# Kernel optimization log

Hardware: AMD Instinct MI355X
Metric: run time of the kernel (lower is better)

Reference implementation:

```python
import jax, jax.numpy as jnp
import numpy as np

N = 100000   # nodes
E = 1600000  # edges (avg degree 16)
F_IN = 128
H = 128
C = 16


def setup_inputs() -> dict:
    key = jax.random.key(0)
    ks = jax.random.split(key, 13)
    s = 1.0 / np.sqrt(H)
    return {
        "x": jax.random.normal(ks[0], (N, F_IN), jnp.float32),
        "edge_index": jax.random.randint(ks[1], (2, E), 0, N, jnp.int32),
        "edge_weight": jax.random.uniform(ks[2], (E,), jnp.float32),
        "W1": jax.random.normal(ks[3], (F_IN, H), jnp.float32) * s,
        "b1": jnp.zeros((H,), jnp.float32),
        "W2": jax.random.normal(ks[4], (H, H), jnp.float32) * s,
        "b2": jnp.zeros((H,), jnp.float32),
        "Wg": jax.random.normal(ks[5], (H, H), jnp.float32) * s,
        "att_src": jax.random.normal(ks[6], (H,), jnp.float32) * s,
        "att_dst": jax.random.normal(ks[7], (H,), jnp.float32) * s,
        "bg": jnp.zeros((H,), jnp.float32),
        "Wc": jax.random.normal(ks[8], (H, C), jnp.float32) * s,
        "bc": jnp.zeros((C,), jnp.float32),
    }


def reference(x, edge_index, edge_weight, W1, b1, W2, b2, Wg, att_src, att_dst, bg, Wc, bc):
    n = x.shape[0]
    loop = jnp.arange(n, dtype=edge_index.dtype)
    src = jnp.concatenate([edge_index[0], loop])   # self loops (PyG default)
    dst = jnp.concatenate([edge_index[1], loop])
    ew = jnp.concatenate([edge_weight, jnp.ones((n,), x.dtype)])  # loop weight 1

    # GCN normalization: D^{-1/2} A D^{-1/2}, degree on dst with edge weights
    deg = jax.ops.segment_sum(ew, dst, num_segments=n)
    dinv = jnp.where(deg > 0, jax.lax.rsqrt(deg), 0.0)
    norm = dinv[src] * ew * dinv[dst]              # [E+N]

    def gcn(h, W, b):
        h = h @ W                                   # [N,H]
        agg = jax.ops.segment_sum(h[src] * norm[:, None], dst, num_segments=n)
        return agg + b

    h = jax.nn.relu(gcn(x, W1, b1))
    h = jax.nn.relu(gcn(h, W2, b2))                 # dropout inert in eval

    # GATConv, heads=1
    g = h @ Wg                                      # [N,H]
    a = jax.nn.leaky_relu((g @ att_src)[src] + (g @ att_dst)[dst], 0.2)
    amax = jax.ops.segment_max(a, dst, num_segments=n)
    ex = jnp.exp(a - amax[dst])
    denom = jax.ops.segment_sum(ex, dst, num_segments=n)
    alpha = ex / denom[dst]                         # edge softmax per dst
    out = jax.ops.segment_sum(g[src] * alpha[:, None], dst, num_segments=n) + bg
    out = jax.nn.relu(out)
    return out @ Wc + bc
```

## Files before the change

### kernel.cpp

```cpp
#include <hip/hip_runtime.h>
#include <hip/hip_fp16.h>

#define FIN 128
#define HD 128
#define COUT 16

#define SLOT_CAP 48
#define CS_BLOCKS 512
#define CB_SHIFT 9
#define CB_SIZE 512
#define CAP_B 10240
#define GMK_CELLS 64
#define NBINS 49

typedef _Float16 half8 __attribute__((ext_vector_type(8)));
typedef float floatx4 __attribute__((ext_vector_type(4)));

__device__ __forceinline__ float lrelu02(float x) { return x > 0.f ? x : 0.2f * x; }

union U4H8 { uint4 q; __half2 h2[4]; };
union UQH8 { uint4 q; half8 h; _Float16 e[8]; };

__device__ __forceinline__ void h8f(const uint4 q, float* f) {
    U4H8 u; u.q = q;
    float2 a0 = __half22float2(u.h2[0]);
    float2 a1 = __half22float2(u.h2[1]);
    float2 a2 = __half22float2(u.h2[2]);
    float2 a3 = __half22float2(u.h2[3]);
    f[0] = a0.x; f[1] = a0.y; f[2] = a1.x; f[3] = a1.y;
    f[4] = a2.x; f[5] = a2.y; f[6] = a3.x; f[7] = a3.y;
}

__device__ __forceinline__ unsigned fkey(float f) {
    unsigned u = __float_as_uint(f);
    return (u & 0x80000000u) ? ~u : (u | 0x80000000u);
}
__device__ __forceinline__ float funkey(unsigned k) {
    return (k & 0x80000000u) ? __uint_as_float(k ^ 0x80000000u)
                             : __uint_as_float(~k);
}

__global__ void k_setup(const float* __restrict__ W1, const float* __restrict__ W2,
                        const float* __restrict__ Wg, __half* __restrict__ w1z,
                        __half* __restrict__ w2z, __half* __restrict__ wgz,
                        int* __restrict__ cur, unsigned* __restrict__ gmk,
                        int* __restrict__ hist) {
    int b = blockIdx.x;
    if (b < 24) {
        const float* W = (b < 8) ? W1 : (b < 16) ? W2 : Wg;
        __half* outp   = (b < 8) ? w1z : (b < 16) ? w2z : wgz;
        int t = (b & 7) * 256 + threadIdx.x;
        int lane = t & 63;
        int kc = (t >> 6) & 3;
        int nt = t >> 8;
        int kbase = kc * 32 + (lane >> 4) * 8;
        int col = nt * 16 + (lane & 15);
        UQH8 u;
#pragma unroll
        for (int j = 0; j < 8; j++)
            u.e[j] = (_Float16)W[(kbase + j) * 128 + col];
        ((uint4*)outp)[t] = u.q;
    } else {
        cur[threadIdx.x] = 0;
        if (threadIdx.x < 64) hist[threadIdx.x] = 0;
        for (int i = threadIdx.x; i < GMK_CELLS * 16; i += 256)
            gmk[i] = 0u;
    }
}

__device__ __forceinline__
void gemm_body_f32(int blk, const float* __restrict__ A, const __half* __restrict__ Wz,
                   __half* __restrict__ Out, int n) {
    int wave = threadIdx.x >> 6;
    int lane = threadIdx.x & 63;
    int m0 = blk * 64 + wave * 16;
    if (m0 >= n) return;
    int m = lane & 15;
    int quad = lane >> 4;

    half8 a[4];
#pragma unroll
    for (int kc = 0; kc < 4; kc++) {
        const float* p = &A[(size_t)(m0 + m) * 128 + kc * 32 + quad * 8];
        float4 f0 = *(const float4*)p;
        float4 f1 = *(const float4*)(p + 4);
        UQH8 u;
        u.e[0] = (_Float16)f0.x; u.e[1] = (_Float16)f0.y;
        u.e[2] = (_Float16)f0.z; u.e[3] = (_Float16)f0.w;
        u.e[4] = (_Float16)f1.x; u.e[5] = (_Float16)f1.y;
        u.e[6] = (_Float16)f1.z; u.e[7] = (_Float16)f1.w;
        a[kc] = u.h;
    }

    floatx4 acc[8];
#pragma unroll
    for (int nt = 0; nt < 8; nt++) acc[nt] = (floatx4){0.f, 0.f, 0.f, 0.f};

    const uint4* Wv = (const uint4*)Wz;
#pragma unroll
    for (int kc = 0; kc < 4; kc++) {
#pragma unroll
        for (int nt = 0; nt < 8; nt++) {
            UQH8 u;
            u.q = Wv[(nt * 4 + kc) * 64 + lane];
            acc[nt] = __builtin_amdgcn_mfma_f32_16x16x32_f16(a[kc], u.h, acc[nt], 0, 0, 0);
        }
    }
#pragma unroll
    for (int nt = 0; nt < 8; nt++) {
#pragma unroll
        for (int reg = 0; reg < 4; reg++) {
            Out[(size_t)(m0 + quad * 4 + reg) * 128 + nt * 16 + m] =
                __float2half(acc[nt][reg]);
        }
    }
}

__launch_bounds__(256)
__global__ void k_csc_gemm(const int* __restrict__ src, const int* __restrict__ dst,
                           const float* __restrict__ ew, int* __restrict__ cur,
                           int2* __restrict__ coarseBuf, int e,
                           const float* __restrict__ x, const __half* __restrict__ w1z,
                           __half* __restrict__ buf0, int n) {
    __shared__ int lcnt[256], lbase[256], lpos[256];
    if ((int)blockIdx.x < CS_BLOCKS) {
        int tid = threadIdx.x;
        lcnt[tid] = 0; lpos[tid] = 0;
        __syncthreads();
        int chunk = (e + CS_BLOCKS - 1) / CS_BLOCKS;
        int s0 = blockIdx.x * chunk;
        int s1 = min(s0 + chunk, e);
        for (int i = s0 + tid; i < s1; i += 256)
            atomicAdd(&lcnt[dst[i] >> CB_SHIFT], 1);
        __syncthreads();
        if (lcnt[tid] > 0) lbase[tid] = atomicAdd(&cur[tid], lcnt[tid]);
        __syncthreads();
        for (int i = s0 + tid; i < s1; i += 256) {
            int d = dst[i];
            int b = d >> CB_SHIFT;
            int pos = lbase[b] + atomicAdd(&lpos[b], 1);
            if (pos < CAP_B)
                coarseBuf[(size_t)b * CAP_B + pos] =
                    make_int2(((d & (CB_SIZE - 1)) << 17) | src[i], __float_as_int(ew[i]));
        }
    } else {
        gemm_body_f32(blockIdx.x - CS_BLOCKS, x, w1z, buf0, n);
    }
}

__launch_bounds__(512)
__global__ void k_fine(const int2* __restrict__ coarseBuf, const int* __restrict__ cur,
                       int2* __restrict__ slots, int* __restrict__ cnt,
                       float* __restrict__ dinv, int* __restrict__ hist, int n) {
    __shared__ int lcnt[CB_SIZE];
    __shared__ float lsum[CB_SIZE];
    __shared__ int lhist[NBINS];
    int b = blockIdx.x;
    int tid = threadIdx.x;
    if (tid < CB_SIZE) { lcnt[tid] = 0; lsum[tid] = 0.f; }
    if (tid >= CB_SIZE && tid - CB_SIZE < NBINS) lhist[tid - CB_SIZE] = 0;
    if (tid < NBINS && CB_SIZE >= 512) lhist[tid] = 0;
    __syncthreads();
    int ecnt = min(cur[b], CAP_B);
    size_t e0 = (size_t)b * CAP_B;
    for (int e = tid; e < ecnt; e += 512) {
        int2 it = coarseBuf[e0 + e];
        int dl = (it.x >> 17) & (CB_SIZE - 1);
        int srcn = it.x & 0x1FFFF;
        int pos = atomicAdd(&lcnt[dl], 1);
        atomicAdd(&lsum[dl], __int_as_float(it.y));
        if (pos < SLOT_CAP) {
            int node = (b << CB_SHIFT) + dl;
            slots[(size_t)node * SLOT_CAP + pos] = make_int2(srcn, it.y);
        }
    }
    __syncthreads();
    if (tid < CB_SIZE) {
        int node = (b << CB_SHIFT) + tid;
        if (node < n) {
            int c = min(lcnt[tid], SLOT_CAP);
            cnt[node] = c;
            dinv[node] = rsqrtf(1.0f + lsum[tid]);
            atomicAdd(&lhist[c], 1);
        }
    }
    __syncthreads();
    if (tid < NBINS && lhist[tid] > 0) atomicAdd(&hist[tid], lhist[tid]);
}

__global__ void k_prefix(const int* __restrict__ hist, int* __restrict__ binCur) {
    if (threadIdx.x == 0) {
        int acc = 0;
        for (int c = 0; c < NBINS; c++) { binCur[c] = acc; acc += hist[c]; }
    }
}

__launch_bounds__(512)
__global__ void k_permscatter(const int* __restrict__ cnt, int* __restrict__ binCur,
                              int* __restrict__ perm, int n) {
    __shared__ int lh[NBINS], lb[NBINS], lp[NBINS];
    int tid = threadIdx.x;
    if (tid < NBINS) { lh[tid] = 0; lp[tid] = 0; }
    __syncthreads();
    int node = blockIdx.x * 512 + tid;
    int c = -1;
    if (node < n) { c = cnt[node]; atomicAdd(&lh[c], 1); }
    __syncthreads();
    if (tid < NBINS && lh[tid] > 0) lb[tid] = atomicAdd(&binCur[tid], lh[tid]);
    __syncthreads();
    if (node < n) {
        int pos = lb[c] + atomicAdd(&lp[c], 1);
        perm[pos] = node;
    }
}

__device__ __forceinline__
void gather_body(int node, int lane, const int* __restrict__ cnt,
                 const int2* __restrict__ slots, const uint4* __restrict__ tv,
                 const float* __restrict__ dinv, const float* __restrict__ b,
                 float* __restrict__ fout) {
    float dd = dinv[node];
    float sw = dd * dd;
    float acc[8];
    {
        uint4 q = tv[(size_t)node * 16 + lane];
        float f[8]; h8f(q, f);
#pragma unroll
        for (int j = 0; j < 8; j++) acc[j] = f[j] * sw;
    }
    int r0 = (int)((size_t)node * SLOT_CAP);
    int r1 = r0 + cnt[node];
    int e = r0;
    for (; e + 8 <= r1; e += 8) {
        int2 c[8];
        float dv[8];
        uint4 v[8];
#pragma unroll
        for (int j = 0; j < 8; j++) c[j] = slots[e + j];
#pragma unroll
        for (int j = 0; j < 8; j++) dv[j] = dinv[c[j].x];
#pragma unroll
        for (int j = 0; j < 8; j++) v[j] = tv[(size_t)c[j].x * 16 + lane];
#pragma unroll
        for (int j = 0; j < 8; j++) {
            float w = dv[j] * __int_as_float(c[j].y) * dd;
            float f[8]; h8f(v[j], f);
#pragma unroll
            for (int k = 0; k < 8; k++) acc[k] = fmaf(f[k], w, acc[k]);
        }
    }
    for (; e + 2 <= r1; e += 2) {
        int2 c0 = slots[e], c1 = slots[e + 1];
        float dv0 = dinv[c0.x], dv1 = dinv[c1.x];
        uint4 v0 = tv[(size_t)c0.x * 16 + lane];
        uint4 v1 = tv[(size_t)c1.x * 16 + lane];
        float w0 = dv0 * __int_as_float(c0.y) * dd;
        float w1 = dv1 * __int_as_float(c1.y) * dd;
        float f0[8], f1[8]; h8f(v0, f0); h8f(v1, f1);
#pragma unroll
        for (int k = 0; k < 8; k++) acc[k] = fmaf(f0[k], w0, acc[k]);
#pragma unroll
        for (int k = 0; k < 8; k++) acc[k] = fmaf(f1[k], w1, acc[k]);
    }
    if (e < r1) {
        int2 c = slots[e];
        uint4 v = tv[(size_t)c.x * 16 + lane];
        float w = dinv[c.x] * __int_as_float(c.y) * dd;
        float f[8]; h8f(v, f);
#pragma unroll
        for (int k = 0; k < 8; k++) acc[k] = fmaf(f[k], w, acc[k]);
    }
    const float4* b4 = (const float4*)b;
    float4 bb0 = b4[lane * 2], bb1 = b4[lane * 2 + 1];
    fout[0] = fmaxf(acc[0] + bb0.x, 0.f);
    fout[1] = fmaxf(acc[1] + bb0.y, 0.f);
    fout[2] = fmaxf(acc[2] + bb0.z, 0.f);
    fout[3] = fmaxf(acc[3] + bb0.w, 0.f);
    fout[4] = fmaxf(acc[4] + bb1.x, 0.f);
    fout[5] = fmaxf(acc[5] + bb1.y, 0.f);
    fout[6] = fmaxf(acc[6] + bb1.z, 0.f);
    fout[7] = fmaxf(acc[7] + bb1.w, 0.f);
}

template <bool ATTN>
__launch_bounds__(256)
__global__ void k_gather_gemm(const int* __restrict__ cnt, const int2* __restrict__ slots,
                              const __half* __restrict__ t, const float* __restrict__ dinv,
                              const float* __restrict__ b, const __half* __restrict__ Wz,
                              __half* __restrict__ Out, const int* __restrict__ perm,
                              const float* __restrict__ attS, const float* __restrict__ attD,
                              float* __restrict__ as_, float* __restrict__ ad_,
                              unsigned* __restrict__ gmaxKey, int n) {
    __shared__ __half stage[16][136];
    __shared__ float redS[4][16], redD[4][16];
    int tid = threadIdx.x;
    int nl = tid >> 4;
    int lane16 = tid & 15;
    int idx16 = blockIdx.x * 16 + nl;
    int node = (idx16 < n) ? perm[idx16] : -1;

    if (node >= 0) {
        float f[8];
        gather_body(node, lane16, cnt, slots, (const uint4*)t, dinv, b, f);
        UQH8 u;
#pragma unroll
        for (int j = 0; j < 8; j++) u.e[j] = (_Float16)f[j];
        *(uint4*)&stage[nl][lane16 * 8] = u.q;
    } else {
        UQH8 u;
#pragma unroll
        for (int j = 0; j < 8; j++) u.e[j] = (_Float16)0.f;
        *(uint4*)&stage[nl][lane16 * 8] = u.q;
    }
    __syncthreads();

    int wave = tid >> 6;
    int lane = tid & 63;
    int m = lane & 15;
    int quad = lane >> 4;
    int m0 = blockIdx.x * 16;

    half8 a[4];
#pragma unroll
    for (int kc = 0; kc < 4; kc++)
        a[kc] = *(const half8*)&stage[m][kc * 32 + quad * 8];

    floatx4 acc[2];
    acc[0] = (floatx4){0.f, 0.f, 0.f, 0.f};
    acc[1] = (floatx4){0.f, 0.f, 0.f, 0.f};
    const uint4* Wv = (const uint4*)Wz;
#pragma unroll
    for (int t2 = 0; t2 < 2; t2++) {
        int nt = wave * 2 + t2;
#pragma unroll
        for (int kc = 0; kc < 4; kc++) {
            UQH8 u;
            u.q = Wv[(nt * 4 + kc) * 64 + lane];
            acc[t2] = __builtin_amdgcn_mfma_f32_16x16x32_f16(a[kc], u.h, acc[t2], 0, 0, 0);
        }
    }
#pragma unroll
    for (int reg = 0; reg < 4; reg++) {
        int row = m0 + quad * 4 + reg;
        if (row < n) {
            int prow = perm[row];
#pragma unroll
            for (int t2 = 0; t2 < 2; t2++) {
                int col = (wave * 2 + t2) * 16 + m;
                Out[(size_t)prow * 128 + col] = __float2half(acc[t2][reg]);
            }
        }
    }

    if (ATTN) {
        float sv0 = attS[(wave * 2 + 0) * 16 + m], sv1 = attS[(wave * 2 + 1) * 16 + m];
        float dv0 = attD[(wave * 2 + 0) * 16 + m], dv1 = attD[(wave * 2 + 1) * 16 + m];
#pragma unroll
        for (int reg = 0; reg < 4; reg++) {
            float s = acc[0][reg] * sv0 + acc[1][reg] * sv1;
            float d = acc[0][reg] * dv0 + acc[1][reg] * dv1;
#pragma unroll
            for (int k = 8; k >= 1; k >>= 1) {
                s += __shfl_xor(s, k, 64);
                d += __shfl_xor(d, k, 64);
            }
            if (m == 0) {
                redS[wave][quad * 4 + reg] = s;
                redD[wave][quad * 4 + reg] = d;
            }
        }
        __syncthreads();
        if (tid < 16) {
            int nd = m0 + tid;
            unsigned key = 0u;
            if (nd < n) {
                float sv = redS[0][tid] + redS[1][tid] + redS[2][tid] + redS[3][tid];
                float dv = redD[0][tid] + redD[1][tid] + redD[2][tid] + redD[3][tid];
                int pn = perm[nd];
                as_[pn] = sv;
                ad_[pn] = dv;
                key = fkey(sv);
            }
#pragma unroll
            for (int k = 8; k >= 1; k >>= 1) {
                unsigned o = (unsigned)__shfl_xor((int)key, k, 64);
                key = key > o ? key : o;
            }
            if (tid == 0)
                atomicMax(&gmaxKey[(blockIdx.x & (GMK_CELLS - 1)) << 4], key);
        }
    }
}

__launch_bounds__(256)
__global__ void k_gat_final(const int* __restrict__ cnt, const int2* __restrict__ slots,
                            const __half* __restrict__ g, const float* __restrict__ as_,
                            const float* __restrict__ ad_,
                            const unsigned* __restrict__ gmaxKey,
                            const int* __restrict__ perm,
                            const float* __restrict__ bg,
                            const float* __restrict__ Wc, const float* __restrict__ bc,
                            float* __restrict__ out, int n) {
    __shared__ float Wcs[128 * 16];
    __shared__ float bcs[16];
    __shared__ float stage[16][136];
    __shared__ float gmaxS;
    int tid = threadIdx.x;
    for (int i = tid; i < 128 * 16; i += 256) Wcs[i] = Wc[i];
    if (tid < 16) bcs[tid] = bc[tid];

    if (tid < 64) {
        unsigned k = gmaxKey[tid << 4];
#pragma unroll
        for (int d = 32; d >= 1; d >>= 1) {
            unsigned o = (unsigned)__shfl_xor((int)k, d, 64);
            k = k > o ? k : o;
        }
        if (tid == 0) gmaxS = funkey(k);
    }
    __syncthreads();
    float gmax = gmaxS;

    int idx = blockIdx.x * 256 + tid;
    int lidx = idx >> 4;
    int node = (lidx < n) ? perm[lidx] : -1;
    int lane = idx & 15;
    int nl = tid >> 4;

    if (node >= 0) {
        int r0 = (int)((size_t)node * SLOT_CAP);
        int r1 = r0 + cnt[node];
        float ad_d = ad_[node];
        float c = lrelu02(gmax + ad_d);
        const uint4* gv = (const uint4*)g;
        float ex = __expf(lrelu02(as_[node] + ad_d) - c);
        float den = ex;
        float acc[8];
        {
            uint4 q = gv[(size_t)node * 16 + lane];
            float f[8]; h8f(q, f);
#pragma unroll
            for (int j = 0; j < 8; j++) acc[j] = ex * f[j];
        }
        int e = r0;
        for (; e + 8 <= r1; e += 8) {
            int s[8];
            float av[8];
            uint4 u[8];
#pragma unroll
            for (int j = 0; j < 8; j++) s[j] = slots[e + j].x;
#pragma unroll
            for (int j = 0; j < 8; j++) av[j] = as_[s[j]];
#pragma unroll
            for (int j = 0; j < 8; j++) u[j] = gv[(size_t)s[j] * 16 + lane];
#pragma unroll
            for (int j = 0; j < 8; j++) {
                float w = __expf(lrelu02(av[j] + ad_d) - c);
                den += w;
                float f[8]; h8f(u[j], f);
#pragma unroll
                for (int k = 0; k < 8; k++) acc[k] = fmaf(f[k], w, acc[k]);
            }
        }
        for (; e + 2 <= r1; e += 2) {
            int s0 = slots[e].x, s1 = slots[e + 1].x;
            uint4 u0 = gv[(size_t)s0 * 16 + lane];
            uint4 u1 = gv[(size_t)s1 * 16 + lane];
            float w0 = __expf(lrelu02(as_[s0] + ad_d) - c);
            float w1 = __expf(lrelu02(as_[s1] + ad_d) - c);
            den += w0 + w1;
            float f0[8], f1[8]; h8f(u0, f0); h8f(u1, f1);
#pragma unroll
            for (int k = 0; k < 8; k++) acc[k] = fmaf(f0[k], w0, acc[k]);
#pragma unroll
            for (int k = 0; k < 8; k++) acc[k] = fmaf(f1[k], w1, acc[k]);
        }
        if (e < r1) {
            int s = slots[e].x;
            uint4 u = gv[(size_t)s * 16 + lane];
            float w = __expf(lrelu02(as_[s] + ad_d) - c);
            den += w;
            float f[8]; h8f(u, f);
#pragma unroll
            for (int k = 0; k < 8; k++) acc[k] = fmaf(f[k], w, acc[k]);
        }
        float inv = 1.0f / den;
        const float4* bg4 = (const float4*)bg;
        float4 b0 = bg4[lane * 2], b1 = bg4[lane * 2 + 1];
        float* sp = &stage[nl][lane * 8];
        sp[0] = fmaxf(acc[0] * inv + b0.x, 0.f);
        sp[1] = fmaxf(acc[1] * inv + b0.y, 0.f);
        sp[2] = fmaxf(acc[2] * inv + b0.z, 0.f);
        sp[3] = fmaxf(acc[3] * inv + b0.w, 0.f);
        sp[4] = fmaxf(acc[4] * inv + b1.x, 0.f);
        sp[5] = fmaxf(acc[5] * inv + b1.y, 0.f);
        sp[6] = fmaxf(acc[6] * inv + b1.z, 0.f);
        sp[7] = fmaxf(acc[7] * inv + b1.w, 0.f);
    }
    __syncthreads();
    int nl2 = tid >> 4;
    int col = tid & 15;
    int oidx = blockIdx.x * 16 + nl2;
    if (oidx >= n) return;
    int onode = perm[oidx];
    float accp = bcs[col];
    const float* sp = stage[nl2];
#pragma unroll 8
    for (int k = 0; k < 128; k++)
        accp = fmaf(sp[k], Wcs[k * 16 + col], accp);
    out[(size_t)onode * 16 + col] = accp;
}

extern "C" void kernel_launch(void* const* d_in, const int* in_sizes, int n_in,
                              void* d_out, int out_size, void* d_ws, size_t ws_size,
                              hipStream_t stream) {
    const float* x      = (const float*)d_in[0];
    const int*   eidx   = (const int*)d_in[1];
    const float* ew     = (const float*)d_in[2];
    const float* W1     = (const float*)d_in[3];
    const float* b1     = (const float*)d_in[4];
    const float* W2     = (const float*)d_in[5];
    const float* b2     = (const float*)d_in[6];
    const float* Wg     = (const float*)d_in[7];
    const float* attS   = (const float*)d_in[8];
    const float* attD   = (const float*)d_in[9];
    const float* bg     = (const float*)d_in[10];
    const float* Wc     = (const float*)d_in[11];
    const float* bc     = (const float*)d_in[12];

    const int N = in_sizes[0] / FIN;
    const int E = in_sizes[2];
    const int* src = eidx;
    const int* dst = eidx + E;
    const int NB = (N + CB_SIZE - 1) >> CB_SHIFT;

    char* base = (char*)d_ws;
    size_t off = 0;
    auto carve = [&](size_t bytes) {
        char* q = base + off;
        off = (off + bytes + 255) & ~(size_t)255;
        return (void*)q;
    };
    int*    cnt       = (int*)carve((size_t)N * 4);
    int*    cur       = (int*)carve(256 * 4);
    unsigned* gmk     = (unsigned*)carve((size_t)GMK_CELLS * 16 * 4);
    int*    hist      = (int*)carve(64 * 4);
    int*    binCur    = (int*)carve(64 * 4);
    int*    perm      = (int*)carve((size_t)N * 4);
    int2*   coarseBuf = (int2*)carve((size_t)NB * CAP_B * 8);
    int2*   slots     = (int2*)carve((size_t)N * SLOT_CAP * 8);
    float*  dinv      = (float*)carve((size_t)N * 4);
    float*  as_       = (float*)carve((size_t)N * 4);
    float*  ad_       = (float*)carve((size_t)N * 4);
    __half* w1z       = (__half*)carve((size_t)128 * 128 * 2);
    __half* w2z       = (__half*)carve((size_t)128 * 128 * 2);
    __half* wgz       = (__half*)carve((size_t)128 * 128 * 2);
    __half* buf0      = (__half*)carve((size_t)N * 128 * 2);
    __half* buf1      = (__half*)carve((size_t)N * 128 * 2);

    const int B = 256;
    dim3 blk(B);
    int fusedGrid = (N + 15) / 16;
    int gemmGrid = (N + 63) / 64;

    k_setup<<<25, blk, 0, stream>>>(W1, W2, Wg, w1z, w2z, wgz, cur, gmk, hist);
    k_csc_gemm<<<CS_BLOCKS + gemmGrid, blk, 0, stream>>>(src, dst, ew, cur, coarseBuf, E,
                                                         x, w1z, buf0, N);
    k_fine<<<NB, dim3(512), 0, stream>>>(coarseBuf, cur, slots, cnt, dinv, hist, N);
    k_prefix<<<1, dim3(64), 0, stream>>>(hist, binCur);
    k_permscatter<<<NB, dim3(512), 0, stream>>>(cnt, binCur, perm, N);

    k_gather_gemm<false><<<fusedGrid, blk, 0, stream>>>(cnt, slots, buf0, dinv, b1, w2z,
                                                        buf1, perm, nullptr, nullptr,
                                                        nullptr, nullptr, nullptr, N);
    k_gather_gemm<true><<<fusedGrid, blk, 0, stream>>>(cnt, slots, buf1, dinv, b2, wgz,
                                                       buf0, perm, attS, attD, as_, ad_,
                                                       gmk, N);
    k_gat_final<<<fusedGrid, blk, 0, stream>>>(cnt, slots, buf0, as_, ad_, gmk, perm, bg,
                                               Wc, bc, (float*)d_out, N);
}
```

Baseline: 414.4 us.

## Stage coarse bucket scatter in shared memory for coalesced global writes

The coarse CSC binning phase now processes each block's edge chunk in tiles of SBUF_CAP edges. Each tile is bucket-sorted locally using a shared-memory prefix scan, then written to coarseBuf in sorted order, so consecutive threads write contiguous positions of the same bucket instead of scattering randomly. The cost is extra shared memory (about 31 KB), several more barriers per tile, and a log-step scan, which may lower occupancy for the co-scheduled GEMM blocks that share this kernel. The lhist initialization in k_fine is also simplified without changing behavior.

```diff
diff --git a/kernel.cpp b/kernel.cpp
--- a/kernel.cpp
+++ b/kernel.cpp
@@ -12,6 +12,7 @@
 #define CAP_B 10240
 #define GMK_CELLS 64
 #define NBINS 49
+#define SBUF_CAP 3136
 
 typedef _Float16 half8 __attribute__((ext_vector_type(8)));
 typedef float floatx4 __attribute__((ext_vector_type(4)));
@@ -122,26 +123,49 @@
                            int2* __restrict__ coarseBuf, int e,
                            const float* __restrict__ x, const __half* __restrict__ w1z,
                            __half* __restrict__ buf0, int n) {
-    __shared__ int lcnt[256], lbase[256], lpos[256];
+    __shared__ int2 sbuf[SBUF_CAP];
+    __shared__ unsigned short sbufb[SBUF_CAP];
+    __shared__ int lcnt[256], lofs[256], lpos[256], lbase[256];
     if ((int)blockIdx.x < CS_BLOCKS) {
         int tid = threadIdx.x;
-        lcnt[tid] = 0; lpos[tid] = 0;
-        __syncthreads();
         int chunk = (e + CS_BLOCKS - 1) / CS_BLOCKS;
         int s0 = blockIdx.x * chunk;
         int s1 = min(s0 + chunk, e);
-        for (int i = s0 + tid; i < s1; i += 256)
-            atomicAdd(&lcnt[dst[i] >> CB_SHIFT], 1);
-        __syncthreads();
-        if (lcnt[tid] > 0) lbase[tid] = atomicAdd(&cur[tid], lcnt[tid]);
-        __syncthreads();
-        for (int i = s0 + tid; i < s1; i += 256) {
-            int d = dst[i];
-            int b = d >> CB_SHIFT;
-            int pos = lbase[b] + atomicAdd(&lpos[b], 1);
-            if (pos < CAP_B)
-                coarseBuf[(size_t)b * CAP_B + pos] =
-                    make_int2(((d & (CB_SIZE - 1)) << 17) | src[i], __float_as_int(ew[i]));
+        for (int t0 = s0; t0 < s1; t0 += SBUF_CAP) {
+            int t1 = min(t0 + SBUF_CAP, s1);
+            lcnt[tid] = 0; lpos[tid] = 0;
+            __syncthreads();
+            for (int i = t0 + tid; i < t1; i += 256)
+                atomicAdd(&lcnt[dst[i] >> CB_SHIFT], 1);
+            __syncthreads();
+            lofs[tid] = lcnt[tid];
+            __syncthreads();
+            for (int d = 1; d < 256; d <<= 1) {
+                int v = (tid >= d) ? lofs[tid - d] : 0;
+                __syncthreads();
+                lofs[tid] += v;
+                __syncthreads();
+            }
+            if (lcnt[tid] > 0) lbase[tid] = atomicAdd(&cur[tid], lcnt[tid]);
+            __syncthreads();
+            for (int i = t0 + tid; i < t1; i += 256) {
+                int d = dst[i];
+                int b = d >> CB_SHIFT;
+                int p = (lofs[b] - lcnt[b]) + atomicAdd(&lpos[b], 1);
+                sbuf[p] = make_int2(((d & (CB_SIZE - 1)) << 17) | src[i],
+                                    __float_as_int(ew[i]));
+                sbufb[p] = (unsigned short)b;
+            }
+            __syncthreads();
+            int total = t1 - t0;
+            for (int t = tid; t < total; t += 256) {
+                int b = sbufb[t];
+                int local = t - (lofs[b] - lcnt[b]);
+                int gpos = lbase[b] + local;
+                if (gpos < CAP_B)
+                    coarseBuf[(size_t)b * CAP_B + gpos] = sbuf[t];
+            }
+            __syncthreads();
         }
     } else {
         gemm_body_f32(blockIdx.x - CS_BLOCKS, x, w1z, buf0, n);
@@ -158,8 +182,7 @@
     int b = blockIdx.x;
     int tid = threadIdx.x;
     if (tid < CB_SIZE) { lcnt[tid] = 0; lsum[tid] = 0.f; }
-    if (tid >= CB_SIZE && tid - CB_SIZE < NBINS) lhist[tid - CB_SIZE] = 0;
-    if (tid < NBINS && CB_SIZE >= 512) lhist[tid] = 0;
+    if (tid < NBINS) lhist[tid] = 0;
     __syncthreads();
     int ecnt = min(cur[b], CAP_B);
     size_t e0 = (size_t)b * CAP_B;
```

Result: faster. 406.0 us, median of 2 (-2.0%).
